# Kernel optimization log

Hardware: AMD Instinct MI355X
Metric: run time of the kernel (lower is better)

The kernel has to match this reference:

```python
import jax, jax.numpy as jnp
import numpy as np

NU, NI, D, NNZ = 80000, 40000, 128, 2000000
EPS = 1e-12


def _spmm(dst, src, vals, x, n):
    # sum_e vals[e] * x[src[e]] scattered to dst[e]; A is [n, x.shape[0]] in COO.
    return jax.ops.segment_sum(vals[:, None] * x[src], dst, num_segments=n)


def setup_inputs() -> dict:
    key = jax.random.key(0)
    ks = jax.random.split(key, 24)
    limit = float(np.sqrt(6.0 / (D + D)))  # xavier_uniform
    inp = {
        'user_embedding': jax.random.normal(ks[0], (NU, D), jnp.float32),
        'item_embedding': jax.random.normal(ks[1], (NI, D), jnp.float32),
        'uu_embed0': jax.random.normal(ks[2], (NU, D), jnp.float32),
        'ii_embed0': jax.random.normal(ks[3], (NI, D), jnp.float32),
        'uu_embed1': jax.random.normal(ks[4], (NU, D), jnp.float32),
        'ii_embed1': jax.random.normal(ks[5], (NI, D), jnp.float32),
        'uu_embed2': jax.random.normal(ks[6], (NU, D), jnp.float32),
        'ii_embed2': jax.random.normal(ks[7], (NI, D), jnp.float32),
        'u_w': jax.random.uniform(ks[8], (D, D), jnp.float32, -limit, limit),
        'i_w': jax.random.uniform(ks[9], (D, D), jnp.float32, -limit, limit),
    }
    for b in range(4):
        inp[f'rows{b}'] = jax.random.randint(ks[10 + 3 * b], (NNZ,), 0, NU, jnp.int32)
        inp[f'cols{b}'] = jax.random.randint(ks[11 + 3 * b], (NNZ,), 0, NI, jnp.int32)
        inp[f'vals{b}'] = jax.random.uniform(ks[12 + 3 * b], (NNZ,), jnp.float32)
    return inp


def reference(user_embedding, item_embedding, uu_embed0, ii_embed0, uu_embed1,
              ii_embed1, uu_embed2, ii_embed2, u_w, i_w,
              rows0, cols0, vals0, rows1, cols1, vals1,
              rows2, cols2, vals2, rows3, cols3, vals3):
    nu, ni = user_embedding.shape[0], item_embedding.shape[0]
    # behavior 0 = click, 1 = fav, 2 = cart, 3 = buy
    u0 = _spmm(rows0, cols0, vals0, ii_embed0, nu)
    i0 = _spmm(cols0, rows0, vals0, uu_embed0, ni)
    u1 = _spmm(rows1, cols1, vals1, ii_embed1, nu)
    i1 = _spmm(cols1, rows1, vals1, uu_embed1, ni)
    u2 = _spmm(rows2, cols2, vals2, ii_embed2, nu)
    i2 = _spmm(cols2, rows2, vals2, uu_embed2, ni)
    u3 = _spmm(rows3, cols3, vals3, item_embedding, nu)
    i3 = _spmm(cols3, rows3, vals3, user_embedding, ni)
    user_embeddings = jnp.stack([u0, u1, u2, u3], axis=0)  # [4, NU, D]
    item_embeddings = jnp.stack([i0, i1, i2, i3], axis=0)  # [4, NI, D]
    user_out = jax.nn.sigmoid(jnp.mean(user_embeddings, axis=0) @ u_w)
    item_out = jax.nn.sigmoid(jnp.mean(item_embeddings, axis=0) @ i_w)
    # F.normalize default: L2 over dim=1 (the node axis of the stacked tensor)
    def l2n(x):
        return x / jnp.maximum(jnp.linalg.norm(x, axis=1, keepdims=True), EPS)
    return (user_out, item_out, l2n(user_embeddings), l2n(item_embeddings),
            u0, i0, u1, i1, u2, i2)
```

## Files before the change

### kernel.cpp

```cpp
#include <hip/hip_runtime.h>

#define NU 80000
#define NI 40000
#define DD 128
#define NNZ_E 2000000
#define EPSN 1e-12f
#define BWROWS 256
#define NBU 313
#define NBI 157
#define NBPAD 320
#define BSTRIDE 336
#define BIN_E 8192
#define S2CAP 16384

struct EdgePtrs { const int* rows[4]; const int* cols[4]; const float* vals[4]; };

__device__ inline unsigned short f2bf(float f) {
  unsigned int u = __float_as_uint(f);
  u += 0x7FFFu + ((u >> 16) & 1u);
  return (unsigned short)(u >> 16);
}

__global__ __launch_bounds__(256) void conv_k(const float* __restrict__ src,
                                              unsigned short* __restrict__ dst, int n4) {
  int stride = blockDim.x * gridDim.x;
  for (int i = blockIdx.x * blockDim.x + threadIdx.x; i < n4; i += stride) {
    float4 f = ((const float4*)src)[i];
    ushort4 h;
    h.x = f2bf(f.x); h.y = f2bf(f.y); h.z = f2bf(f.z); h.w = f2bf(f.w);
    ((ushort4*)dst)[i] = h;
  }
}

__global__ __launch_bounds__(256) void histB_k(EdgePtrs ep, int* cntA) {
  int b = blockIdx.y;
  const int* __restrict__ rows = ep.rows[b];
  const int* __restrict__ cols = ep.cols[b];
  __shared__ int lh[NBU + NBI];
  for (int i = threadIdx.x; i < NBU + NBI; i += blockDim.x) lh[i] = 0;
  __syncthreads();
  int stride = blockDim.x * gridDim.x;
  for (int e = blockIdx.x * blockDim.x + threadIdx.x; e < NNZ_E; e += stride) {
    atomicAdd(&lh[rows[e] >> 8], 1);
    atomicAdd(&lh[NBU + (cols[e] >> 8)], 1);
  }
  __syncthreads();
  int* cu = cntA + (b * 2 + 0) * NBPAD;
  int* ci = cntA + (b * 2 + 1) * NBPAD;
  for (int i = threadIdx.x; i < NBU + NBI; i += blockDim.x) {
    int v = lh[i];
    if (v) {
      if (i < NBU) atomicAdd(&cu[i], v);
      else atomicAdd(&ci[i - NBU], v);
    }
  }
}

__global__ __launch_bounds__(512) void scanb_k(const int* cntA, int* baseA, int* gcurA) {
  __shared__ int wsums[9];
  int a = blockIdx.x;
  int dir = a & 1;
  int n = dir ? NBI : NBU;
  const int* cnt = cntA + a * NBPAD;
  int* base = baseA + a * BSTRIDE;
  int* gcur = gcurA + a * NBPAD;
  int t = threadIdx.x, lane = t & 63, w = t >> 6;
  int v = (t < n) ? cnt[t] : 0;
  int s = v;
  #pragma unroll
  for (int off = 1; off < 64; off <<= 1) {
    int x = __shfl_up(s, off);
    if (lane >= off) s += x;
  }
  if (lane == 63) wsums[w] = s;
  __syncthreads();
  if (t == 0) {
    int run = 0;
    for (int k = 0; k < 8; k++) { int x = wsums[k]; wsums[k] = run; run += x; }
    wsums[8] = run;
  }
  __syncthreads();
  int ex = wsums[w] + s - v;
  if (t < n) { base[t] = ex; gcur[t] = ex; }
  if (t == 0) base[n] = wsums[8];
}

__global__ __launch_bounds__(512) void bin_k(EdgePtrs ep, int b0, int* gcurA, int2* binned) {
  __shared__ int2 stage[BIN_E];
  __shared__ int lh[NBPAD], lscan[NBPAD], lcur[NBPAD], gpos[NBPAD];
  __shared__ int wsums[9];
  int dir = blockIdx.y, j = blockIdx.z, b = b0 + j;
  int NB = dir ? NBI : NBU;
  const int* __restrict__ dst = dir ? ep.cols[b] : ep.rows[b];
  const int* __restrict__ src = dir ? ep.rows[b] : ep.cols[b];
  const float* __restrict__ vals = ep.vals[b];
  int* gcur = gcurA + (b * 2 + dir) * NBPAD;
  int2* out = binned + ((size_t)j * 2 + dir) * NNZ_E;
  int t = threadIdx.x;
  int e0 = blockIdx.x * BIN_E;
  int nh = min(BIN_E, NNZ_E - e0);
  for (int i = t; i < NBPAD; i += 512) lh[i] = 0;
  __syncthreads();
  for (int i = t; i < nh; i += 512) atomicAdd(&lh[dst[e0 + i] >> 8], 1);
  __syncthreads();
  {
    int lane = t & 63, w = t >> 6;
    int v = (t < NB) ? lh[t] : 0;
    int s = v;
    #pragma unroll
    for (int off = 1; off < 64; off <<= 1) {
      int x = __shfl_up(s, off);
      if (lane >= off) s += x;
    }
    if (lane == 63) wsums[w] = s;
    __syncthreads();
    if (t == 0) {
      int run = 0;
      for (int k = 0; k < 8; k++) { int x = wsums[k]; wsums[k] = run; run += x; }
      wsums[8] = run;
    }
    __syncthreads();
    int ex = wsums[w] + s - v;
    if (t < NB) { lscan[t] = ex; lcur[t] = ex; gpos[t] = atomicAdd(&gcur[t], v); }
  }
  __syncthreads();
  for (int i = t; i < nh; i += 512) {
    int d = dst[e0 + i], s = src[e0 + i];
    int k = d >> 8;
    int pos = atomicAdd(&lcur[k], 1);
    stage[pos] = make_int2(s | ((d & 255) << 17), __float_as_int(vals[e0 + i]));
  }
  __syncthreads();
  int w = t >> 6, lane = t & 63;
  for (int k = w; k < NB; k += 8) {
    int c = lh[k];
    const int2* sp = stage + lscan[k];
    int2* gp = out + gpos[k];
    for (int i = lane; i < c; i += 64) gp[i] = sp[i];
  }
}

__global__ __launch_bounds__(512) void sort3_k(int* rpU, int* rpI, int b0,
                                               const int* baseA, int2* binned) {
  __shared__ int2 stage[S2CAP];
  __shared__ int lh[256];
  __shared__ int excl[257];
  __shared__ int lcur[256];
  __shared__ int wsums[5];
  int gb = blockIdx.x;
  int j = gb / (NBU + NBI);
  int r = gb - j * (NBU + NBI);
  int dir = (r >= NBU) ? 1 : 0;
  int k = dir ? (r - NBU) : r;
  int b = b0 + j;
  int n = dir ? NI : NU;
  int* rp = dir ? (rpI + (size_t)b * (NI + 1)) : (rpU + (size_t)b * (NU + 1));
  const int* base = baseA + (b * 2 + dir) * BSTRIDE;
  int2* bb = binned + ((size_t)j * 2 + dir) * NNZ_E;
  int row0 = k << 8;
  int nrows = min(BWROWS, n - row0);
  int base0 = base[k];
  int tot = base[k + 1] - base0;
  int t = threadIdx.x;
  if (t < 256) lh[t] = 0;
  __syncthreads();
  for (int i = t; i < tot; i += 512) atomicAdd(&lh[(bb[base0 + i].x >> 17) & 255], 1);
  __syncthreads();
  int v = 0, s = 0;
  if (t < 256) {
    int lane = t & 63, w = t >> 6;
    v = lh[t]; s = v;
    #pragma unroll
    for (int off = 1; off < 64; off <<= 1) {
      int x = __shfl_up(s, off);
      if (lane >= off) s += x;
    }
    if (lane == 63) wsums[w] = s;
  }
  __syncthreads();
  if (t == 0) {
    int run = 0;
    for (int q = 0; q < 4; q++) { int x = wsums[q]; wsums[q] = run; run += x; }
    wsums[4] = run;
  }
  __syncthreads();
  if (t < 256) {
    int ex = wsums[t >> 6] + s - v;
    excl[t] = ex; lcur[t] = ex;
  }
  if (t == 0) excl[256] = wsums[4];
  __syncthreads();
  if (t <= nrows) rp[row0 + t] = base0 + excl[t];
  for (int i = t; i < tot; i += 512) {
    int2 p = bb[base0 + i];
    int ld = (p.x >> 17) & 255;
    int pos = atomicAdd(&lcur[ld], 1);
    stage[pos] = make_int2(p.x & 0x1FFFF, p.y);
  }
  __syncthreads();
  for (int i = t; i < tot; i += 512) bb[base0 + i] = stage[i];
}

__global__ __launch_bounds__(256) void gather_k(const int* __restrict__ rp, const int2* __restrict__ pairs,
                                                const void* __restrict__ xt, int isbf,
                                                float* __restrict__ out1, float* __restrict__ out2,
                                                int nrows) {
  int gid = blockIdx.x * 8 + (threadIdx.x >> 5);
  int lane = threadIdx.x & 31;
  int tot = gridDim.x * 8;
  for (int r = gid; r < nrows; r += tot) {
    int beg = rp[r], end = rp[r + 1];
    float4 a0 = make_float4(0.f, 0.f, 0.f, 0.f);
    float4 a1 = make_float4(0.f, 0.f, 0.f, 0.f);
    int e = beg;
    if (isbf) {
      const ushort4* __restrict__ x4 = (const ushort4*)xt;
      for (; e + 3 < end; e += 4) {
        int2 p0 = pairs[e], p1 = pairs[e + 1], p2 = pairs[e + 2], p3 = pairs[e + 3];
        ushort4 h0 = x4[(size_t)p0.x * 32 + lane];
        ushort4 h1 = x4[(size_t)p1.x * 32 + lane];
        ushort4 h2 = x4[(size_t)p2.x * 32 + lane];
        ushort4 h3 = x4[(size_t)p3.x * 32 + lane];
        float v0 = __int_as_float(p0.y), v1 = __int_as_float(p1.y);
        float v2 = __int_as_float(p2.y), v3 = __int_as_float(p3.y);
        a0.x += v0 * __uint_as_float((unsigned)h0.x << 16);
        a0.y += v0 * __uint_as_float((unsigned)h0.y << 16);
        a0.z += v0 * __uint_as_float((unsigned)h0.z << 16);
        a0.w += v0 * __uint_as_float((unsigned)h0.w << 16);
        a1.x += v1 * __uint_as_float((unsigned)h1.x << 16);
        a1.y += v1 * __uint_as_float((unsigned)h1.y << 16);
        a1.z += v1 * __uint_as_float((unsigned)h1.z << 16);
        a1.w += v1 * __uint_as_float((unsigned)h1.w << 16);
        a0.x += v2 * __uint_as_float((unsigned)h2.x << 16);
        a0.y += v2 * __uint_as_float((unsigned)h2.y << 16);
        a0.z += v2 * __uint_as_float((unsigned)h2.z << 16);
        a0.w += v2 * __uint_as_float((unsigned)h2.w << 16);
        a1.x += v3 * __uint_as_float((unsigned)h3.x << 16);
        a1.y += v3 * __uint_as_float((unsigned)h3.y << 16);
        a1.z += v3 * __uint_as_float((unsigned)h3.z << 16);
        a1.w += v3 * __uint_as_float((unsigned)h3.w << 16);
      }
      for (; e < end; e++) {
        int2 p = pairs[e];
        ushort4 h = x4[(size_t)p.x * 32 + lane];
        float v = __int_as_float(p.y);
        a0.x += v * __uint_as_float((unsigned)h.x << 16);
        a0.y += v * __uint_as_float((unsigned)h.y << 16);
        a0.z += v * __uint_as_float((unsigned)h.z << 16);
        a0.w += v * __uint_as_float((unsigned)h.w << 16);
      }
    } else {
      const float4* __restrict__ x4 = (const float4*)xt;
      for (; e + 3 < end; e += 4) {
        int2 p0 = pairs[e], p1 = pairs[e + 1], p2 = pairs[e + 2], p3 = pairs[e + 3];
        float4 x0 = x4[(size_t)p0.x * 32 + lane];
        float4 x1 = x4[(size_t)p1.x * 32 + lane];
        float4 x2 = x4[(size_t)p2.x * 32 + lane];
        float4 x3 = x4[(size_t)p3.x * 32 + lane];
        float v0 = __int_as_float(p0.y), v1 = __int_as_float(p1.y);
        float v2 = __int_as_float(p2.y), v3 = __int_as_float(p3.y);
        a0.x += v0 * x0.x; a0.y += v0 * x0.y; a0.z += v0 * x0.z; a0.w += v0 * x0.w;
        a1.x += v1 * x1.x; a1.y += v1 * x1.y; a1.z += v1 * x1.z; a1.w += v1 * x1.w;
        a0.x += v2 * x2.x; a0.y += v2 * x2.y; a0.z += v2 * x2.z; a0.w += v2 * x2.w;
        a1.x += v3 * x3.x; a1.y += v3 * x3.y; a1.z += v3 * x3.z; a1.w += v3 * x3.w;
      }
      for (; e < end; e++) {
        int2 p = pairs[e];
        float4 xv = x4[(size_t)p.x * 32 + lane];
        float v = __int_as_float(p.y);
        a0.x += v * xv.x; a0.y += v * xv.y; a0.z += v * xv.z; a0.w += v * xv.w;
      }
    }
    float4 res = make_float4(a0.x + a1.x, a0.y + a1.y, a0.z + a1.z, a0.w + a1.w);
    ((float4*)out1)[(size_t)r * 32 + lane] = res;
    if (out2) ((float4*)out2)[(size_t)r * 32 + lane] = res;
  }
}

__global__ __launch_bounds__(256) void gemm_sig_k(const float* __restrict__ x, size_t sstride,
                                                  const float* __restrict__ W, float* __restrict__ out,
                                                  int n) {
  __shared__ float wl[DD * DD];
  __shared__ float rl[8][DD];
  for (int i = threadIdx.x; i < DD * DD / 4; i += blockDim.x)
    ((float4*)wl)[i] = ((const float4*)W)[i];
  int c = threadIdx.x & 127;
  int g = threadIdx.x >> 7;
  int row0 = blockIdx.x * 64;
  for (int rr = 0; rr < 64; rr += 8) {
    int rbase = row0 + rr;
    __syncthreads();
    for (int i = threadIdx.x; i < 8 * DD; i += blockDim.x) {
      int lr = i >> 7, lc = i & 127;
      int r = rbase + lr;
      float m = 0.f;
      if (r < n) {
        size_t off = (size_t)r * DD + lc;
        m = 0.25f * (x[off] + x[off + sstride] + x[off + 2 * sstride] + x[off + 3 * sstride]);
      }
      rl[lr][lc] = m;
    }
    __syncthreads();
    float acc0 = 0.f, acc1 = 0.f, acc2 = 0.f, acc3 = 0.f;
    #pragma unroll 4
    for (int k = 0; k < DD; k++) {
      float wv = wl[k * DD + c];
      acc0 += rl[g * 4 + 0][k] * wv;
      acc1 += rl[g * 4 + 1][k] * wv;
      acc2 += rl[g * 4 + 2][k] * wv;
      acc3 += rl[g * 4 + 3][k] * wv;
    }
    float accs[4] = {acc0, acc1, acc2, acc3};
    for (int jj = 0; jj < 4; jj++) {
      int r = rbase + g * 4 + jj;
      if (r < n) out[(size_t)r * DD + c] = 1.f / (1.f + __expf(-accs[jj]));
    }
  }
}

__global__ __launch_bounds__(256) void colsq_k(const float* __restrict__ base, size_t sstride, int n,
                                               float* __restrict__ sums) {
  int b = blockIdx.y;
  const float* x = base + (size_t)b * sstride;
  int c = threadIdx.x & 127;
  int rh = threadIdx.x >> 7;
  float acc = 0.f;
  for (int r = blockIdx.x * 2 + rh; r < n; r += gridDim.x * 2) {
    float v = x[(size_t)r * DD + c];
    acc += v * v;
  }
  __shared__ float red[256];
  red[threadIdx.x] = acc;
  __syncthreads();
  if (threadIdx.x < 128) atomicAdd(&sums[b * DD + threadIdx.x], red[threadIdx.x] + red[threadIdx.x + 128]);
}

__global__ void inv_k(const float* __restrict__ sums, float* __restrict__ inv, int n) {
  int i = blockIdx.x * blockDim.x + threadIdx.x;
  if (i < n) inv[i] = 1.f / fmaxf(sqrtf(sums[i]), EPSN);
}

__global__ __launch_bounds__(256) void scale_k(float* __restrict__ base, size_t slice_f4,
                                               const float* __restrict__ inv) {
  int b = blockIdx.y;
  float4* b4 = (float4*)base + (size_t)b * slice_f4;
  const float4* inv4 = (const float4*)inv + (size_t)b * 32;
  size_t stride = (size_t)blockDim.x * gridDim.x;
  for (size_t i = (size_t)blockIdx.x * blockDim.x + threadIdx.x; i < slice_f4; i += stride) {
    float4 s = inv4[i & 31];
    float4 v = b4[i];
    v.x *= s.x; v.y *= s.y; v.z *= s.z; v.w *= s.w;
    b4[i] = v;
  }
}

extern "C" void kernel_launch(void* const* d_in, const int* in_sizes, int n_in,
                              void* d_out, int out_size, void* d_ws, size_t ws_size,
                              hipStream_t stream) {
  const float* user_emb = (const float*)d_in[0];
  const float* item_emb = (const float*)d_in[1];
  const float* uu[4] = {(const float*)d_in[2], (const float*)d_in[4], (const float*)d_in[6], user_emb};
  const float* ii[4] = {(const float*)d_in[3], (const float*)d_in[5], (const float*)d_in[7], item_emb};
  const float* u_w = (const float*)d_in[8];
  const float* i_w = (const float*)d_in[9];
  EdgePtrs ep;
  for (int b = 0; b < 4; b++) {
    ep.rows[b] = (const int*)d_in[10 + 3 * b];
    ep.cols[b] = (const int*)d_in[11 + 3 * b];
    ep.vals[b] = (const float*)d_in[12 + 3 * b];
  }

  float* out = (float*)d_out;
  float* user_out = out;
  float* item_out = out + (size_t)NU * DD;
  float* l2nU = item_out + (size_t)NI * DD;
  float* l2nI = l2nU + (size_t)4 * NU * DD;
  float* u_slot[3];
  float* i_slot[3];
  {
    float* p = l2nI + (size_t)4 * NI * DD;
    for (int b = 0; b < 3; b++) {
      u_slot[b] = p; p += (size_t)NU * DD;
      i_slot[b] = p; p += (size_t)NI * DD;
    }
  }

  const size_t binsl = (size_t)2 * NNZ_E * 8;
  const size_t item_bf_sz = (size_t)4 * NI * DD * 2;
  const size_t user_bf_sz = (size_t)4 * NU * DD * 2;
  const size_t smalls = 8u << 20;

  int batchB; bool bfI, bfU;
  if (ws_size >= 4 * binsl + item_bf_sz + user_bf_sz + smalls) { batchB = 4; bfI = bfU = true; }
  else if (ws_size >= 2 * binsl + item_bf_sz + user_bf_sz + smalls) { batchB = 2; bfI = bfU = true; }
  else if (ws_size >= binsl + item_bf_sz + user_bf_sz + smalls) { batchB = 1; bfI = bfU = true; }
  else if (ws_size >= binsl + item_bf_sz + smalls) { batchB = 1; bfI = true; bfU = false; }
  else { batchB = 1; bfI = bfU = false; }

  char* w = (char*)d_ws;
  auto alloc = [&](size_t bytes) {
    char* r = w;
    w += (bytes + 255) & ~(size_t)255;
    return r;
  };
  int2* binned = (int2*)alloc((size_t)batchB * binsl);
  unsigned short* itemB = bfI ? (unsigned short*)alloc(item_bf_sz) : nullptr;
  unsigned short* userB = bfU ? (unsigned short*)alloc(user_bf_sz) : nullptr;
  int* cntA = (int*)alloc(4 * 2 * NBPAD * 4);
  int* baseA = (int*)alloc(4 * 2 * BSTRIDE * 4);
  int* gcurA = (int*)alloc(4 * 2 * NBPAD * 4);
  int* rpU = (int*)alloc((size_t)4 * (NU + 1) * 4);
  int* rpI = (int*)alloc((size_t)4 * (NI + 1) * 4);
  float* colsums = (float*)alloc(8 * DD * 4);
  float* invs = (float*)alloc(8 * DD * 4);

  if (bfI)
    for (int b = 0; b < 4; b++)
      conv_k<<<512, 256, 0, stream>>>(ii[b], itemB + (size_t)b * NI * DD, NI * DD / 4);
  if (bfU)
    for (int b = 0; b < 4; b++)
      conv_k<<<512, 256, 0, stream>>>(uu[b], userB + (size_t)b * NU * DD, NU * DD / 4);

  hipMemsetAsync(cntA, 0, 4 * 2 * NBPAD * 4, stream);
  histB_k<<<dim3(256, 4), 256, 0, stream>>>(ep, cntA);
  scanb_k<<<8, 512, 0, stream>>>(cntA, baseA, gcurA);

  const int nchunks = (NNZ_E + BIN_E - 1) / BIN_E;
  for (int b0 = 0; b0 < 4; b0 += batchB) {
    bin_k<<<dim3(nchunks, 2, batchB), 512, 0, stream>>>(ep, b0, gcurA, binned);
    sort3_k<<<batchB * (NBU + NBI), 512, 0, stream>>>(rpU, rpI, b0, baseA, binned);
    for (int j = 0; j < batchB; j++) {
      int b = b0 + j;
      const void* xt0 = bfI ? (const void*)(itemB + (size_t)b * NI * DD) : (const void*)ii[b];
      const void* xt1 = bfU ? (const void*)(userB + (size_t)b * NU * DD) : (const void*)uu[b];
      gather_k<<<10000, 256, 0, stream>>>(rpU + (size_t)b * (NU + 1),
                                          binned + ((size_t)j * 2 + 0) * NNZ_E, xt0, bfI ? 1 : 0,
                                          l2nU + (size_t)b * NU * DD, (b < 3) ? u_slot[b] : nullptr, NU);
      gather_k<<<5000, 256, 0, stream>>>(rpI + (size_t)b * (NI + 1),
                                         binned + ((size_t)j * 2 + 1) * NNZ_E, xt1, bfU ? 1 : 0,
                                         l2nI + (size_t)b * NI * DD, (b < 3) ? i_slot[b] : nullptr, NI);
    }
  }

  gemm_sig_k<<<NU / 64, 256, 0, stream>>>(l2nU, (size_t)NU * DD, u_w, user_out, NU);
  gemm_sig_k<<<NI / 64, 256, 0, stream>>>(l2nI, (size_t)NI * DD, i_w, item_out, NI);

  hipMemsetAsync(colsums, 0, 8 * DD * 4, stream);
  colsq_k<<<dim3(512, 4), 256, 0, stream>>>(l2nU, (size_t)NU * DD, NU, colsums);
  colsq_k<<<dim3(512, 4), 256, 0, stream>>>(l2nI, (size_t)NI * DD, NI, colsums + 4 * DD);
  inv_k<<<4, 256, 0, stream>>>(colsums, invs, 8 * DD);
  scale_k<<<dim3(1024, 4), 256, 0, stream>>>(l2nU, (size_t)NU * 32, invs);
  scale_k<<<dim3(1024, 4), 256, 0, stream>>>(l2nI, (size_t)NI * 32, invs + 4 * DD);
}
```

Measured before the change: 1.398 ms.

## Fuse four behavior gathers with mean and column-norm reduction into one kernel

Adds a gather kernel that processes all four behaviors per row in one pass, writing each result, the four-way mean, and per-column sum-of-squares partials (reduced in shared memory, then atomically added into replicated global slots). This removes the separate re-reads of the stacked embeddings by the GEMM and the column-norm kernels, and the GEMM now reads a precomputed mean buffer. It also merges the two scale launches into one and reorders the bf16 conversions after binning. The cost is an extra mean buffer and more atomics, and the fused path only runs when the workspace fits all four batches. The unrolled loop in the fallback gather is removed.

```diff
diff --git a/kernel.cpp b/kernel.cpp
--- a/kernel.cpp
+++ b/kernel.cpp
@@ -12,8 +12,20 @@
 #define BSTRIDE 336
 #define BIN_E 8192
 #define S2CAP 16384
+#define NREP 4
 
 struct EdgePtrs { const int* rows[4]; const int* cols[4]; const float* vals[4]; };
+
+struct GM4 {
+  const int* rp[4];
+  const int2* pairs[4];
+  const unsigned short* xt[4];
+  float* out[4];
+  float* dup[4];
+  float* meanb;
+  float* colsums;
+  int cbase;
+};
 
 __device__ inline unsigned short f2bf(float f) {
   unsigned int u = __float_as_uint(f);
@@ -201,20 +213,22 @@
   for (int i = t; i < tot; i += 512) bb[base0 + i] = stage[i];
 }
 
-__global__ __launch_bounds__(256) void gather_k(const int* __restrict__ rp, const int2* __restrict__ pairs,
-                                                const void* __restrict__ xt, int isbf,
-                                                float* __restrict__ out1, float* __restrict__ out2,
-                                                int nrows) {
+__global__ __launch_bounds__(256) void gather4_k(GM4 gm, int nrows, int ngroups) {
   int gid = blockIdx.x * 8 + (threadIdx.x >> 5);
   int lane = threadIdx.x & 31;
-  int tot = gridDim.x * 8;
-  for (int r = gid; r < nrows; r += tot) {
-    int beg = rp[r], end = rp[r + 1];
-    float4 a0 = make_float4(0.f, 0.f, 0.f, 0.f);
-    float4 a1 = make_float4(0.f, 0.f, 0.f, 0.f);
-    int e = beg;
-    if (isbf) {
-      const ushort4* __restrict__ x4 = (const ushort4*)xt;
+  int t = threadIdx.x;
+  float4 sq0 = make_float4(0.f,0.f,0.f,0.f), sq1 = sq0, sq2 = sq0, sq3 = sq0;
+  for (int r = gid; r < nrows; r += ngroups) {
+    float4 mean = make_float4(0.f,0.f,0.f,0.f);
+    #pragma unroll
+    for (int b = 0; b < 4; b++) {
+      const int* rp = gm.rp[b];
+      const int2* __restrict__ pairs = gm.pairs[b];
+      const ushort4* __restrict__ x4 = (const ushort4*)gm.xt[b];
+      int beg = rp[r], end = rp[r + 1];
+      float4 a0 = make_float4(0.f,0.f,0.f,0.f);
+      float4 a1 = make_float4(0.f,0.f,0.f,0.f);
+      int e = beg;
       for (; e + 3 < end; e += 4) {
         int2 p0 = pairs[e], p1 = pairs[e + 1], p2 = pairs[e + 2], p3 = pairs[e + 3];
         ushort4 h0 = x4[(size_t)p0.x * 32 + lane];
@@ -249,21 +263,59 @@
         a0.z += v * __uint_as_float((unsigned)h.z << 16);
         a0.w += v * __uint_as_float((unsigned)h.w << 16);
       }
+      float4 res = make_float4(a0.x + a1.x, a0.y + a1.y, a0.z + a1.z, a0.w + a1.w);
+      ((float4*)gm.out[b])[(size_t)r * 32 + lane] = res;
+      if (gm.dup[b]) ((float4*)gm.dup[b])[(size_t)r * 32 + lane] = res;
+      mean.x += res.x; mean.y += res.y; mean.z += res.z; mean.w += res.w;
+      float4* sqp = (b == 0) ? &sq0 : (b == 1) ? &sq1 : (b == 2) ? &sq2 : &sq3;
+      sqp->x += res.x * res.x; sqp->y += res.y * res.y;
+      sqp->z += res.z * res.z; sqp->w += res.w * res.w;
+    }
+    mean.x *= 0.25f; mean.y *= 0.25f; mean.z *= 0.25f; mean.w *= 0.25f;
+    ((float4*)gm.meanb)[(size_t)r * 32 + lane] = mean;
+  }
+  __shared__ float csq[512];
+  csq[t] = 0.f; csq[t + 256] = 0.f;
+  __syncthreads();
+  int cb = lane * 4;
+  atomicAdd(&csq[0 * 128 + cb + 0], sq0.x); atomicAdd(&csq[0 * 128 + cb + 1], sq0.y);
+  atomicAdd(&csq[0 * 128 + cb + 2], sq0.z); atomicAdd(&csq[0 * 128 + cb + 3], sq0.w);
+  atomicAdd(&csq[1 * 128 + cb + 0], sq1.x); atomicAdd(&csq[1 * 128 + cb + 1], sq1.y);
+  atomicAdd(&csq[1 * 128 + cb + 2], sq1.z); atomicAdd(&csq[1 * 128 + cb + 3], sq1.w);
+  atomicAdd(&csq[2 * 128 + cb + 0], sq2.x); atomicAdd(&csq[2 * 128 + cb + 1], sq2.y);
+  atomicAdd(&csq[2 * 128 + cb + 2], sq2.z); atomicAdd(&csq[2 * 128 + cb + 3], sq2.w);
+  atomicAdd(&csq[3 * 128 + cb + 0], sq3.x); atomicAdd(&csq[3 * 128 + cb + 1], sq3.y);
+  atomicAdd(&csq[3 * 128 + cb + 2], sq3.z); atomicAdd(&csq[3 * 128 + cb + 3], sq3.w);
+  __syncthreads();
+  float* dst = gm.colsums + (blockIdx.x & (NREP - 1)) * 1024 + gm.cbase;
+  atomicAdd(&dst[t], csq[t]);
+  atomicAdd(&dst[t + 256], csq[t + 256]);
+}
+
+__global__ __launch_bounds__(256) void gather_k(const int* __restrict__ rp, const int2* __restrict__ pairs,
+                                                const void* __restrict__ xt, int isbf,
+                                                float* __restrict__ out1, float* __restrict__ out2,
+                                                int nrows) {
+  int gid = blockIdx.x * 8 + (threadIdx.x >> 5);
+  int lane = threadIdx.x & 31;
+  int tot = gridDim.x * 8;
+  for (int r = gid; r < nrows; r += tot) {
+    int beg = rp[r], end = rp[r + 1];
+    float4 a0 = make_float4(0.f, 0.f, 0.f, 0.f);
+    int e = beg;
+    if (isbf) {
+      const ushort4* __restrict__ x4 = (const ushort4*)xt;
+      for (; e < end; e++) {
+        int2 p = pairs[e];
+        ushort4 h = x4[(size_t)p.x * 32 + lane];
+        float v = __int_as_float(p.y);
+        a0.x += v * __uint_as_float((unsigned)h.x << 16);
+        a0.y += v * __uint_as_float((unsigned)h.y << 16);
+        a0.z += v * __uint_as_float((unsigned)h.z << 16);
+        a0.w += v * __uint_as_float((unsigned)h.w << 16);
+      }
     } else {
       const float4* __restrict__ x4 = (const float4*)xt;
-      for (; e + 3 < end; e += 4) {
-        int2 p0 = pairs[e], p1 = pairs[e + 1], p2 = pairs[e + 2], p3 = pairs[e + 3];
-        float4 x0 = x4[(size_t)p0.x * 32 + lane];
-        float4 x1 = x4[(size_t)p1.x * 32 + lane];
-        float4 x2 = x4[(size_t)p2.x * 32 + lane];
-        float4 x3 = x4[(size_t)p3.x * 32 + lane];
-        float v0 = __int_as_float(p0.y), v1 = __int_as_float(p1.y);
-        float v2 = __int_as_float(p2.y), v3 = __int_as_float(p3.y);
-        a0.x += v0 * x0.x; a0.y += v0 * x0.y; a0.z += v0 * x0.z; a0.w += v0 * x0.w;
-        a1.x += v1 * x1.x; a1.y += v1 * x1.y; a1.z += v1 * x1.z; a1.w += v1 * x1.w;
-        a0.x += v2 * x2.x; a0.y += v2 * x2.y; a0.z += v2 * x2.z; a0.w += v2 * x2.w;
-        a1.x += v3 * x3.x; a1.y += v3 * x3.y; a1.z += v3 * x3.z; a1.w += v3 * x3.w;
-      }
       for (; e < end; e++) {
         int2 p = pairs[e];
         float4 xv = x4[(size_t)p.x * 32 + lane];
@@ -271,9 +323,44 @@
         a0.x += v * xv.x; a0.y += v * xv.y; a0.z += v * xv.z; a0.w += v * xv.w;
       }
     }
-    float4 res = make_float4(a0.x + a1.x, a0.y + a1.y, a0.z + a1.z, a0.w + a1.w);
-    ((float4*)out1)[(size_t)r * 32 + lane] = res;
-    if (out2) ((float4*)out2)[(size_t)r * 32 + lane] = res;
+    ((float4*)out1)[(size_t)r * 32 + lane] = a0;
+    if (out2) ((float4*)out2)[(size_t)r * 32 + lane] = a0;
+  }
+}
+
+__global__ __launch_bounds__(256) void gemm_sig_m(const float* __restrict__ mean,
+                                                  const float* __restrict__ W, float* __restrict__ out,
+                                                  int n) {
+  __shared__ float wl[DD * DD];
+  __shared__ float rl[8][DD];
+  for (int i = threadIdx.x; i < DD * DD / 4; i += blockDim.x)
+    ((float4*)wl)[i] = ((const float4*)W)[i];
+  int c = threadIdx.x & 127;
+  int g = threadIdx.x >> 7;
+  int row0 = blockIdx.x * 64;
+  for (int rr = 0; rr < 64; rr += 8) {
+    int rbase = row0 + rr;
+    __syncthreads();
+    for (int i = threadIdx.x; i < 8 * DD; i += blockDim.x) {
+      int lr = i >> 7, lc = i & 127;
+      int r = rbase + lr;
+      rl[lr][lc] = (r < n) ? mean[(size_t)r * DD + lc] : 0.f;
+    }
+    __syncthreads();
+    float acc0 = 0.f, acc1 = 0.f, acc2 = 0.f, acc3 = 0.f;
+    #pragma unroll 4
+    for (int k = 0; k < DD; k++) {
+      float wv = wl[k * DD + c];
+      acc0 += rl[g * 4 + 0][k] * wv;
+      acc1 += rl[g * 4 + 1][k] * wv;
+      acc2 += rl[g * 4 + 2][k] * wv;
+      acc3 += rl[g * 4 + 3][k] * wv;
+    }
+    float accs[4] = {acc0, acc1, acc2, acc3};
+    for (int jj = 0; jj < 4; jj++) {
+      int r = rbase + g * 4 + jj;
+      if (r < n) out[(size_t)r * DD + c] = 1.f / (1.f + __expf(-accs[jj]));
+    }
   }
 }
 
@@ -335,18 +422,25 @@
   if (threadIdx.x < 128) atomicAdd(&sums[b * DD + threadIdx.x], red[threadIdx.x] + red[threadIdx.x + 128]);
 }
 
-__global__ void inv_k(const float* __restrict__ sums, float* __restrict__ inv, int n) {
+__global__ void inv_k(const float* __restrict__ sums, float* __restrict__ inv, int n, int nrep) {
   int i = blockIdx.x * blockDim.x + threadIdx.x;
-  if (i < n) inv[i] = 1.f / fmaxf(sqrtf(sums[i]), EPSN);
-}
-
-__global__ __launch_bounds__(256) void scale_k(float* __restrict__ base, size_t slice_f4,
-                                               const float* __restrict__ inv) {
-  int b = blockIdx.y;
-  float4* b4 = (float4*)base + (size_t)b * slice_f4;
-  const float4* inv4 = (const float4*)inv + (size_t)b * 32;
+  if (i < n) {
+    float s = 0.f;
+    for (int r = 0; r < nrep; r++) s += sums[r * 1024 + i];
+    inv[i] = 1.f / fmaxf(sqrtf(s), EPSN);
+  }
+}
+
+__global__ __launch_bounds__(256) void scaleall_k(float* __restrict__ l2nU, float* __restrict__ l2nI,
+                                                  const float* __restrict__ invs) {
+  int y = blockIdx.y;
+  float4* b4;
+  size_t slice;
+  if (y < 4) { b4 = (float4*)l2nU + (size_t)y * NU * 32; slice = (size_t)NU * 32; }
+  else { b4 = (float4*)l2nI + (size_t)(y - 4) * NI * 32; slice = (size_t)NI * 32; }
+  const float4* inv4 = (const float4*)invs + (size_t)y * 32;
   size_t stride = (size_t)blockDim.x * gridDim.x;
-  for (size_t i = (size_t)blockIdx.x * blockDim.x + threadIdx.x; i < slice_f4; i += stride) {
+  for (size_t i = (size_t)blockIdx.x * blockDim.x + threadIdx.x; i < slice; i += stride) {
     float4 s = inv4[i & 31];
     float4 v = b4[i];
     v.x *= s.x; v.y *= s.y; v.z *= s.z; v.w *= s.w;
@@ -388,10 +482,11 @@
   const size_t binsl = (size_t)2 * NNZ_E * 8;
   const size_t item_bf_sz = (size_t)4 * NI * DD * 2;
   const size_t user_bf_sz = (size_t)4 * NU * DD * 2;
+  const size_t mean_sz = (size_t)(NU + NI) * DD * 4;
   const size_t smalls = 8u << 20;
 
   int batchB; bool bfI, bfU;
-  if (ws_size >= 4 * binsl + item_bf_sz + user_bf_sz + smalls) { batchB = 4; bfI = bfU = true; }
+  if (ws_size >= 4 * binsl + item_bf_sz + user_bf_sz + mean_sz + smalls) { batchB = 4; bfI = bfU = true; }
   else if (ws_size >= 2 * binsl + item_bf_sz + user_bf_sz + smalls) { batchB = 2; bfI = bfU = true; }
   else if (ws_size >= binsl + item_bf_sz + user_bf_sz + smalls) { batchB = 1; bfI = bfU = true; }
   else if (ws_size >= binsl + item_bf_sz + smalls) { batchB = 1; bfI = true; bfU = false; }
@@ -406,49 +501,85 @@
   int2* binned = (int2*)alloc((size_t)batchB * binsl);
   unsigned short* itemB = bfI ? (unsigned short*)alloc(item_bf_sz) : nullptr;
   unsigned short* userB = bfU ? (unsigned short*)alloc(user_bf_sz) : nullptr;
+  float* meanU = nullptr;
+  float* meanI = nullptr;
+  if (batchB == 4) {
+    meanU = (float*)alloc((size_t)NU * DD * 4);
+    meanI = (float*)alloc((size_t)NI * DD * 4);
+  }
   int* cntA = (int*)alloc(4 * 2 * NBPAD * 4);
   int* baseA = (int*)alloc(4 * 2 * BSTRIDE * 4);
   int* gcurA = (int*)alloc(4 * 2 * NBPAD * 4);
   int* rpU = (int*)alloc((size_t)4 * (NU + 1) * 4);
   int* rpI = (int*)alloc((size_t)4 * (NI + 1) * 4);
-  float* colsums = (float*)alloc(8 * DD * 4);
+  float* colsums = (float*)alloc(NREP * 1024 * 4);
   float* invs = (float*)alloc(8 * DD * 4);
-
-  if (bfI)
-    for (int b = 0; b < 4; b++)
-      conv_k<<<512, 256, 0, stream>>>(ii[b], itemB + (size_t)b * NI * DD, NI * DD / 4);
-  if (bfU)
-    for (int b = 0; b < 4; b++)
-      conv_k<<<512, 256, 0, stream>>>(uu[b], userB + (size_t)b * NU * DD, NU * DD / 4);
 
   hipMemsetAsync(cntA, 0, 4 * 2 * NBPAD * 4, stream);
   histB_k<<<dim3(256, 4), 256, 0, stream>>>(ep, cntA);
   scanb_k<<<8, 512, 0, stream>>>(cntA, baseA, gcurA);
 
   const int nchunks = (NNZ_E + BIN_E - 1) / BIN_E;
-  for (int b0 = 0; b0 < 4; b0 += batchB) {
-    bin_k<<<dim3(nchunks, 2, batchB), 512, 0, stream>>>(ep, b0, gcurA, binned);
-    sort3_k<<<batchB * (NBU + NBI), 512, 0, stream>>>(rpU, rpI, b0, baseA, binned);
-    for (int j = 0; j < batchB; j++) {
-      int b = b0 + j;
-      const void* xt0 = bfI ? (const void*)(itemB + (size_t)b * NI * DD) : (const void*)ii[b];
-      const void* xt1 = bfU ? (const void*)(userB + (size_t)b * NU * DD) : (const void*)uu[b];
-      gather_k<<<10000, 256, 0, stream>>>(rpU + (size_t)b * (NU + 1),
-                                          binned + ((size_t)j * 2 + 0) * NNZ_E, xt0, bfI ? 1 : 0,
-                                          l2nU + (size_t)b * NU * DD, (b < 3) ? u_slot[b] : nullptr, NU);
-      gather_k<<<5000, 256, 0, stream>>>(rpI + (size_t)b * (NI + 1),
-                                         binned + ((size_t)j * 2 + 1) * NNZ_E, xt1, bfU ? 1 : 0,
-                                         l2nI + (size_t)b * NI * DD, (b < 3) ? i_slot[b] : nullptr, NI);
-    }
-  }
-
-  gemm_sig_k<<<NU / 64, 256, 0, stream>>>(l2nU, (size_t)NU * DD, u_w, user_out, NU);
-  gemm_sig_k<<<NI / 64, 256, 0, stream>>>(l2nI, (size_t)NI * DD, i_w, item_out, NI);
-
-  hipMemsetAsync(colsums, 0, 8 * DD * 4, stream);
-  colsq_k<<<dim3(512, 4), 256, 0, stream>>>(l2nU, (size_t)NU * DD, NU, colsums);
-  colsq_k<<<dim3(512, 4), 256, 0, stream>>>(l2nI, (size_t)NI * DD, NI, colsums + 4 * DD);
-  inv_k<<<4, 256, 0, stream>>>(colsums, invs, 8 * DD);
-  scale_k<<<dim3(1024, 4), 256, 0, stream>>>(l2nU, (size_t)NU * 32, invs);
-  scale_k<<<dim3(1024, 4), 256, 0, stream>>>(l2nI, (size_t)NI * 32, invs + 4 * DD);
-}
+
+  if (batchB == 4) {
+    bin_k<<<dim3(nchunks, 2, 4), 512, 0, stream>>>(ep, 0, gcurA, binned);
+    sort3_k<<<4 * (NBU + NBI), 512, 0, stream>>>(rpU, rpI, 0, baseA, binned);
+    for (int b = 0; b < 4; b++)
+      conv_k<<<512, 256, 0, stream>>>(ii[b], itemB + (size_t)b * NI * DD, NI * DD / 4);
+    for (int b = 0; b < 4; b++)
+      conv_k<<<512, 256, 0, stream>>>(uu[b], userB + (size_t)b * NU * DD, NU * DD / 4);
+    hipMemsetAsync(colsums, 0, NREP * 1024 * 4, stream);
+
+    GM4 gmU, gmI;
+    for (int b = 0; b < 4; b++) {
+      gmU.rp[b] = rpU + (size_t)b * (NU + 1);
+      gmU.pairs[b] = binned + ((size_t)b * 2 + 0) * NNZ_E;
+      gmU.xt[b] = itemB + (size_t)b * NI * DD;
+      gmU.out[b] = l2nU + (size_t)b * NU * DD;
+      gmU.dup[b] = (b < 3) ? u_slot[b] : nullptr;
+      gmI.rp[b] = rpI + (size_t)b * (NI + 1);
+      gmI.pairs[b] = binned + ((size_t)b * 2 + 1) * NNZ_E;
+      gmI.xt[b] = userB + (size_t)b * NU * DD;
+      gmI.out[b] = l2nI + (size_t)b * NI * DD;
+      gmI.dup[b] = (b < 3) ? i_slot[b] : nullptr;
+    }
+    gmU.meanb = meanU; gmU.colsums = colsums; gmU.cbase = 0;
+    gmI.meanb = meanI; gmI.colsums = colsums; gmI.cbase = 4 * DD;
+    gather4_k<<<2500, 256, 0, stream>>>(gmU, NU, 2500 * 8);
+    gather4_k<<<1250, 256, 0, stream>>>(gmI, NI, 1250 * 8);
+
+    inv_k<<<4, 256, 0, stream>>>(colsums, invs, 8 * DD, NREP);
+    gemm_sig_m<<<NU / 64, 256, 0, stream>>>(meanU, u_w, user_out, NU);
+    gemm_sig_m<<<NI / 64, 256, 0, stream>>>(meanI, i_w, item_out, NI);
+    scaleall_k<<<dim3(1024, 8), 256, 0, stream>>>(l2nU, l2nI, invs);
+  } else {
+    if (bfI)
+      for (int b = 0; b < 4; b++)
+        conv_k<<<512, 256, 0, stream>>>(ii[b], itemB + (size_t)b * NI * DD, NI * DD / 4);
+    if (bfU)
+      for (int b = 0; b < 4; b++)
+        conv_k<<<512, 256, 0, stream>>>(uu[b], userB + (size_t)b * NU * DD, NU * DD / 4);
+    for (int b0 = 0; b0 < 4; b0 += batchB) {
+      bin_k<<<dim3(nchunks, 2, batchB), 512, 0, stream>>>(ep, b0, gcurA, binned);
+      sort3_k<<<batchB * (NBU + NBI), 512, 0, stream>>>(rpU, rpI, b0, baseA, binned);
+      for (int j = 0; j < batchB; j++) {
+        int b = b0 + j;
+        const void* xt0 = bfI ? (const void*)(itemB + (size_t)b * NI * DD) : (const void*)ii[b];
+        const void* xt1 = bfU ? (const void*)(userB + (size_t)b * NU * DD) : (const void*)uu[b];
+        gather_k<<<10000, 256, 0, stream>>>(rpU + (size_t)b * (NU + 1),
+                                            binned + ((size_t)j * 2 + 0) * NNZ_E, xt0, bfI ? 1 : 0,
+                                            l2nU + (size_t)b * NU * DD, (b < 3) ? u_slot[b] : nullptr, NU);
+        gather_k<<<5000, 256, 0, stream>>>(rpI + (size_t)b * (NI + 1),
+                                           binned + ((size_t)j * 2 + 1) * NNZ_E, xt1, bfU ? 1 : 0,
+                                           l2nI + (size_t)b * NI * DD, (b < 3) ? i_slot[b] : nullptr, NI);
+      }
+    }
+    gemm_sig_k<<<NU / 64, 256, 0, stream>>>(l2nU, (size_t)NU * DD, u_w, user_out, NU);
+    gemm_sig_k<<<NI / 64, 256, 0, stream>>>(l2nI, (size_t)NI * DD, i_w, item_out, NI);
+    hipMemsetAsync(colsums, 0, NREP * 1024 * 4, stream);
+    colsq_k<<<dim3(512, 4), 256, 0, stream>>>(l2nU, (size_t)NU * DD, NU, colsums);
+    colsq_k<<<dim3(512, 4), 256, 0, stream>>>(l2nI, (size_t)NI * DD, NI, colsums + 4 * DD);
+    inv_k<<<4, 256, 0, stream>>>(colsums, invs, 8 * DD, 1);
+    scaleall_k<<<dim3(1024, 8), 256, 0, stream>>>(l2nU, l2nI, invs);
+  }
+}
```

After: 1.417 ms. Within noise of the previous version (+1.4%).
